# Optimization experiments

Hardware: AMD Instinct MI355X
Metric: run time of the kernel (lower is better)

The kernel has to match this reference:

```python
import jax, jax.numpy as jnp
import numpy as np

N = 100000      # nodes
E = 1600000     # edges
D_IN = 128
D_OUT = 64
D_EDGE = 2
NEG_SLOPE = 0.01  # F.leaky_relu default


def setup_inputs() -> dict:
    key = jax.random.key(0)
    ks = jax.random.split(key, 8)
    h = jax.random.normal(ks[0], (N, D_IN), dtype=jnp.float32)
    e = jax.random.normal(ks[1], (E, D_EDGE), dtype=jnp.float32)
    src = jax.random.randint(ks[2], (E,), 0, N, dtype=jnp.int32)
    dst = jax.random.randint(ks[3], (E,), 0, N, dtype=jnp.int32)
    # learned params (torch Linear stores [out, in]; y = x @ W.T)
    W_fc = jax.random.normal(ks[4], (D_OUT, D_IN), dtype=jnp.float32) * 0.05
    W_attn = jax.random.normal(ks[5], (1, 2 * D_OUT + D_EDGE), dtype=jnp.float32) * 0.05
    W_edge = jax.random.normal(ks[6], (D_EDGE, D_EDGE), dtype=jnp.float32) * 0.5
    W_e2n = jax.random.normal(ks[7], (D_OUT, D_EDGE), dtype=jnp.float32) * 0.5
    return {"h": h, "e": e, "src": src, "dst": dst,
            "W_fc": W_fc, "W_attn": W_attn, "W_edge": W_edge, "W_e2n": W_e2n}


def reference(h, e, src, dst, W_fc, W_attn, W_edge, W_e2n):
    z = h @ W_fc.T                    # [N, D_OUT]
    ex = e @ W_edge.T                 # [E, D_EDGE]
    ez = ex @ W_e2n.T                 # [E, D_OUT]
    # edge attention logit: attn_fc(concat[z_src, z_dst, ex]) then leaky_relu
    z_src = z[src]                    # [E, D_OUT]
    z_dst = z[dst]                    # [E, D_OUT]
    wa = W_attn[0]                    # [2*D_OUT + D_EDGE]
    a = (z_src @ wa[:D_OUT] + z_dst @ wa[D_OUT:2 * D_OUT]
         + ex @ wa[2 * D_OUT:])       # [E]
    a = jnp.where(a > 0, a, NEG_SLOPE * a)
    # segment softmax over incoming edges of each dst node
    m = jax.ops.segment_max(a, dst, num_segments=N)      # [N]
    m = jnp.where(jnp.isfinite(m), m, 0.0)               # isolated nodes
    a_exp = jnp.exp(a - m[dst])                          # [E]
    denom = jax.ops.segment_sum(a_exp, dst, num_segments=N)  # [N]
    attn = a_exp / denom[dst]                            # [E]
    # h = sum attn * z_src + sum attn * ez  (fused)
    msg = attn[:, None] * (z_src + ez)                   # [E, D_OUT]
    h_out = jax.ops.segment_sum(msg, dst, num_segments=N)  # [N, D_OUT]
    return h_out
```

## Files before the change

### kernel.cpp

```cpp
#include <hip/hip_runtime.h>
#include <hip/hip_fp16.h>
#include <math.h>

#define D_IN 128
#define D_OUT 64
#define NEG_SLOPE 0.01f

#define NBIN 391
#define BSH  8
#define FCAP 6144
#define ECH  2048
#define ETH  512
#define EPT  4
#define CSLOT 48

typedef __attribute__((ext_vector_type(8))) short bf16x8;
typedef __attribute__((ext_vector_type(4))) float f32x4;

static __device__ __forceinline__ unsigned short f2bf(float f) {
    unsigned u = __float_as_uint(f);
    u += 0x7FFFu + ((u >> 16) & 1u);
    return (unsigned short)(u >> 16);
}
static __device__ __forceinline__ float h2f(unsigned bits) {
    __half_raw r; r.x = (unsigned short)bits;
    return __half2float(__half(r));
}
static __device__ __forceinline__ float i8b(unsigned w, int b) {
    return (float)((int)(w << (24 - 8 * b)) >> 24);
}

__global__ __launch_bounds__(256) void k_prep(const float* __restrict__ W_fc,
                                              unsigned short* __restrict__ Wf)
{
    int t = threadIdx.x;
    for (int idx = t; idx < 8192; idx += 256) {
        int j  = idx & 7;
        int l  = (idx >> 3) & 63;
        int ks = (idx >> 9) & 3;
        int ct = idx >> 11;
        int col = ct * 16 + (l & 15);
        int k   = ks * 32 + (l >> 4) * 8 + j;
        Wf[idx] = f2bf(W_fc[col * 128 + k]);
    }
}

__global__ __launch_bounds__(256) void k_z(const float* __restrict__ h,
                                           const unsigned short* __restrict__ Wf,
                                           const float* __restrict__ W_attn,
                                           unsigned* __restrict__ zq,
                                           float* __restrict__ sc1f,
                                           float* __restrict__ s2,
                                           int N)
{
    __shared__ __align__(16) char smem[64 * 68 * 4];
    unsigned short* fr = (unsigned short*)smem;
    float* zt = (float*)smem;

    int t = threadIdx.x;
    int row0 = blockIdx.x * 64;

#pragma unroll
    for (int it = 0; it < 8; ++it) {
        int idx = it * 256 + t;
        int row = idx >> 5, kq = idx & 31;
        int rw = row0 + row;
        float4 v = (rw < N) ? *(const float4*)&h[(size_t)rw * D_IN + kq * 4]
                            : make_float4(0.f, 0.f, 0.f, 0.f);
        ushort4 b;
        b.x = f2bf(v.x); b.y = f2bf(v.y); b.z = f2bf(v.z); b.w = f2bf(v.w);
        int m = kq >> 1;
        int rt = row >> 4, r16 = row & 15;
        int eidx = (rt * 16 + m) * 128 + ((r16 ^ (m & 7)) * 8) + (kq & 1) * 4;
        *(ushort4*)&fr[eidx] = b;
    }
    __syncthreads();

    int w = t >> 6, l = t & 63;
    int kg = l >> 4, r16 = l & 15;

    bf16x8 A[4];
#pragma unroll
    for (int ks = 0; ks < 4; ++ks) {
        int m = ks * 4 + kg;
        A[ks] = *(const bf16x8*)&fr[(w * 16 + m) * 128 + ((r16 ^ (m & 7)) * 8)];
    }
    f32x4 acc[4];
#pragma unroll
    for (int ct = 0; ct < 4; ++ct) {
        acc[ct] = (f32x4){0.f, 0.f, 0.f, 0.f};
#pragma unroll
        for (int ks = 0; ks < 4; ++ks) {
            bf16x8 B = *(const bf16x8*)&Wf[((ct * 4 + ks) * 64 + l) * 8];
            acc[ct] = __builtin_amdgcn_mfma_f32_16x16x32_bf16(A[ks], B, acc[ct], 0, 0, 0);
        }
    }
    __syncthreads();

#pragma unroll
    for (int ct = 0; ct < 4; ++ct)
#pragma unroll
        for (int j = 0; j < 4; ++j)
            zt[(w * 16 + kg * 4 + j) * 68 + ct * 16 + r16] = acc[ct][j];
    __syncthreads();

    int tx = t & 15, ty = t >> 4;
    float a4[4][4];
#pragma unroll
    for (int i = 0; i < 4; i++) {
        float4 vv = *(const float4*)&zt[(ty * 4 + i) * 68 + tx * 4];
        a4[i][0] = vv.x; a4[i][1] = vv.y; a4[i][2] = vv.z; a4[i][3] = vv.w;
    }

#pragma unroll
    for (int i = 0; i < 4; i++) {
        float m = fmaxf(fmaxf(fabsf(a4[i][0]), fabsf(a4[i][1])),
                        fmaxf(fabsf(a4[i][2]), fabsf(a4[i][3])));
#pragma unroll
        for (int msk = 8; msk >= 1; msk >>= 1)
            m = fmaxf(m, __shfl_xor(m, msk));
        float inv = (m > 0.0f) ? 127.0f / m : 0.0f;
        int q0 = __float2int_rn(a4[i][0] * inv);
        int q1 = __float2int_rn(a4[i][1] * inv);
        int q2 = __float2int_rn(a4[i][2] * inv);
        int q3 = __float2int_rn(a4[i][3] * inv);
        q0 = min(127, max(-127, q0)); q1 = min(127, max(-127, q1));
        q2 = min(127, max(-127, q2)); q3 = min(127, max(-127, q3));
        unsigned pk = ((unsigned)(q0 & 255)) | ((unsigned)(q1 & 255) << 8)
                    | ((unsigned)(q2 & 255) << 16) | ((unsigned)(q3 & 255) << 24);
        int row = row0 + ty * 4 + i;
        if (row < N) {
            zq[(size_t)row * 16 + tx] = pk;
            if (tx == 0) sc1f[2 * row] = m * (1.0f / 127.0f);
        }
    }

    float4 wa0 = *(const float4*)&W_attn[tx * 4];
    float4 wa1 = *(const float4*)&W_attn[64 + tx * 4];
#pragma unroll
    for (int i = 0; i < 4; i++) {
        float v1 = a4[i][0] * wa0.x + a4[i][1] * wa0.y + a4[i][2] * wa0.z + a4[i][3] * wa0.w;
        float v2 = a4[i][0] * wa1.x + a4[i][1] * wa1.y + a4[i][2] * wa1.z + a4[i][3] * wa1.w;
#pragma unroll
        for (int msk = 8; msk >= 1; msk >>= 1) {
            v1 += __shfl_xor(v1, msk);
            v2 += __shfl_xor(v2, msk);
        }
        if (tx == 0) {
            int row = row0 + ty * 4 + i;
            if (row < N) { sc1f[2 * row + 1] = v1; s2[row] = v2; }
        }
    }
}

__global__ __launch_bounds__(ETH) void k_edge_bin(const float2* __restrict__ e,
                                                  const int* __restrict__ src,
                                                  const int* __restrict__ dst,
                                                  const float* __restrict__ W_edge,
                                                  const float* __restrict__ W_attn,
                                                  int* __restrict__ fifo_tail,
                                                  unsigned* __restrict__ f0,
                                                  unsigned* __restrict__ f1,
                                                  unsigned char* __restrict__ fD,
                                                  int E)
{
    __shared__ unsigned l0[ECH];
    __shared__ unsigned l1[ECH];
    __shared__ unsigned char ldl[ECH];
    __shared__ unsigned short lbin[ECH];
    __shared__ int cnt[NBIN];
    __shared__ int off[NBIN + 1];
    __shared__ int gbase[NBIN];
    __shared__ int wsum[ETH / 64];

    int t = threadIdx.x;
    int base = blockIdx.x * ECH;

    for (int i = t; i < NBIN; i += ETH) cnt[i] = 0;
    __syncthreads();

    float we0 = W_edge[0], we1 = W_edge[1], we2 = W_edge[2], we3 = W_edge[3];
    float wa0 = W_attn[128], wa1 = W_attn[129];
    float v0c = we0 * wa0 + we2 * wa1;
    float v1c = we1 * wa0 + we3 * wa1;

    unsigned r0[EPT], r1[EPT];
    unsigned char rdl[EPT];
    int rbin[EPT], rrank[EPT];

#pragma unroll
    for (int j = 0; j < EPT; j++) {
        int i = base + j * ETH + t;
        bool ok = (i < E);
        int ii = ok ? i : 0;
        float2 ev = e[ii];
        int s = src[ii], d = dst[ii];
        float a = ev.x * v0c + ev.y * v1c;
        float a2 = fminf(fmaxf(a + 2.0f, 0.0f), 4.0f);
        if (ok) {
            int b = d >> BSH;
            rrank[j] = atomicAdd(&cnt[b], 1);
            rbin[j] = b;
            unsigned pb = __half_as_ushort(__float2half_rn(a2)) & 0x7FFFu;
            r0[j] = ((unsigned)s << 15) | pb;
            unsigned e0b = __half_as_ushort(__float2half_rn(ev.x));
            unsigned e1b = __half_as_ushort(__float2half_rn(ev.y));
            r1[j] = (e0b << 16) | e1b;
            rdl[j] = (unsigned char)(d & 255);
        } else {
            rbin[j] = -1;
        }
    }
    __syncthreads();

    {
        int i0 = 2 * t, i1 = 2 * t + 1;
        int a0 = (i0 < NBIN) ? cnt[i0] : 0;
        int a1 = (i1 < NBIN) ? cnt[i1] : 0;
        int tsum = a0 + a1;
        int lane = t & 63, w = t >> 6;
        int sc = tsum;
#pragma unroll
        for (int o = 1; o < 64; o <<= 1) {
            int u = __shfl_up(sc, o);
            if (lane >= o) sc += u;
        }
        if (lane == 63) wsum[w] = sc;
        __syncthreads();
        int woff = 0;
        for (int ww = 0; ww < w; ww++) woff += wsum[ww];
        int ex = woff + sc - tsum;
        if (i0 <= NBIN) off[i0] = ex;
        if (i1 <= NBIN) off[i1] = ex + a0;
        __syncthreads();
    }

#pragma unroll
    for (int j = 0; j < EPT; j++) {
        if (rbin[j] >= 0) {
            int slot = off[rbin[j]] + rrank[j];
            l0[slot] = r0[j];
            l1[slot] = r1[j];
            ldl[slot] = rdl[j];
            lbin[slot] = (unsigned short)rbin[j];
        }
    }

    for (int i = t; i < NBIN; i += ETH) {
        int c = cnt[i];
        gbase[i] = (c > 0) ? atomicAdd(&fifo_tail[i], c) : 0;
    }
    __syncthreads();

    int total = off[NBIN];
    for (int r = t; r < total; r += ETH) {
        int b = lbin[r];
        int gi = gbase[b] + (r - off[b]);
        if (gi < FCAP) {
            size_t a = (size_t)b * FCAP + gi;
            f0[a] = l0[r];
            f1[a] = l1[r];
            fD[a] = ldl[r];
        }
    }
}

__global__ __launch_bounds__(256) void k_bin2slot(const int* __restrict__ fifo_tail,
                                                  const unsigned* __restrict__ f0,
                                                  const unsigned* __restrict__ f1,
                                                  const unsigned char* __restrict__ fD,
                                                  int* __restrict__ gcur,
                                                  uint2* __restrict__ slots, int N)
{
    __shared__ int cnt[256];
    __shared__ int gb[256];
    __shared__ unsigned short rk[(FCAP + 1) / 2];

    int b = blockIdx.x >> 1;
    int half = blockIdx.x & 1;
    int t = threadIdx.x;

    int cnt0 = fifo_tail[b];
    if (cnt0 > FCAP) cnt0 = FCAP;
    int mid = (cnt0 + 1) >> 1;
    int lo = half ? mid : 0;
    int hi = half ? cnt0 : mid;

    cnt[t] = 0;
    __syncthreads();

    size_t fb = (size_t)b * FCAP;
    for (int idx = lo + t; idx < hi; idx += 256) {
        int dl = fD[fb + idx];
        rk[idx - lo] = (unsigned short)atomicAdd(&cnt[dl], 1);
    }
    __syncthreads();

    {
        int c = cnt[t];
        int node = b * 256 + t;
        gb[t] = (c > 0 && node < N) ? atomicAdd(&gcur[node], c) : 0;
    }
    __syncthreads();

    for (int idx = lo + t; idx < hi; idx += 256) {
        int dl = fD[fb + idx];
        int pos = gb[dl] + (int)rk[idx - lo];
        if (pos < CSLOT) {
            int node = b * 256 + dl;
            slots[(size_t)node * CSLOT + pos] = make_uint2(f0[fb + idx], f1[fb + idx]);
        }
    }
}

__global__ __launch_bounds__(256) void k_node2(const unsigned* __restrict__ zq,
                                               const float2* __restrict__ sc1,
                                               const uint2* __restrict__ slots,
                                               const int* __restrict__ deg,
                                               const float* __restrict__ s2,
                                               const float* __restrict__ W_edge,
                                               const float* __restrict__ W_e2n,
                                               float* __restrict__ out, int N)
{
    int wid = threadIdx.x >> 6, lane = threadIdx.x & 63;
    int hh = lane >> 5, hl = lane & 31;
    int hb = hh << 5;
    int n = blockIdx.x * 8 + wid * 2 + hh;
    bool valid = (n < N);
    int nn = valid ? n : 0;
    size_t base = (size_t)nn * CSLOT;

    uint2 v = slots[base + hl];
    int cnt = deg[nn];
    float s2n = s2[nn] - 2.0f;
    if (!valid) cnt = 0;
    if (cnt > CSLOT) cnt = CSLOT;
    int c32 = cnt < 32 ? cnt : 32;

    unsigned v0 = v.x;
    float p = 0.0f, ps = 0.0f, pe0 = 0.0f, pe1 = 0.0f;
    if (hl < c32) {
        float2 sv = sc1[v.x >> 15];
        float af = h2f(v.x & 0x7FFFu) + sv.y + s2n;
        af = af > 0.0f ? af : NEG_SLOPE * af;
        p = __expf(af);
        ps = p * sv.x;
        pe0 = p * h2f(v.y >> 16);
        pe1 = p * h2f(v.y & 0xFFFFu);
    } else {
        v0 = 0;
    }

    int sub4 = hl & 15, qq = hl >> 4;
    float acc0 = 0.0f, acc1 = 0.0f, acc2 = 0.0f, acc3 = 0.0f;

    int k = 0;
    for (; k + 8 <= c32; k += 8) {
        unsigned aa[4]; float pb[4];
#pragma unroll
        for (int j = 0; j < 4; j++) {
            int kk = hb + k + 2 * j + qq;
            aa[j] = __shfl(v0, kk);
            pb[j] = __shfl(ps, kk);
        }
        unsigned w[4];
#pragma unroll
        for (int j = 0; j < 4; j++)
            w[j] = zq[(size_t)(aa[j] >> 15) * 16 + sub4];
#pragma unroll
        for (int j = 0; j < 4; j++) {
            acc0 = fmaf(pb[j], i8b(w[j], 0), acc0);
            acc1 = fmaf(pb[j], i8b(w[j], 1), acc1);
            acc2 = fmaf(pb[j], i8b(w[j], 2), acc2);
            acc3 = fmaf(pb[j], i8b(w[j], 3), acc3);
        }
    }
    for (; k < c32; k += 2) {
        int kk = hb + k + qq;
        unsigned aa = __shfl(v0, kk);
        float pb = __shfl(ps, kk);
        unsigned w = zq[(size_t)(aa >> 15) * 16 + sub4];
        acc0 = fmaf(pb, i8b(w, 0), acc0);
        acc1 = fmaf(pb, i8b(w, 1), acc1);
        acc2 = fmaf(pb, i8b(w, 2), acc2);
        acc3 = fmaf(pb, i8b(w, 3), acc3);
    }

    if (__any(cnt > 32)) {
        uint2 v2 = slots[base + 32 + (size_t)(hl & 15)];
        unsigned u0 = 0;
        float ps2 = 0.0f;
        if (hl < 16 && 32 + hl < cnt) {
            float2 sv = sc1[v2.x >> 15];
            float af = h2f(v2.x & 0x7FFFu) + sv.y + s2n;
            af = af > 0.0f ? af : NEG_SLOPE * af;
            float p2 = __expf(af);
            ps2 = p2 * sv.x;
            p   += p2;
            pe0 += p2 * h2f(v2.y >> 16);
            pe1 += p2 * h2f(v2.y & 0xFFFFu);
            u0 = v2.x;
        }
        for (int k2 = 0; k2 < 16; k2 += 2) {
            int kk = hb + k2 + qq;
            unsigned aa = __shfl(u0, kk);
            float pb = __shfl(ps2, kk);
            unsigned w = zq[(size_t)(aa >> 15) * 16 + sub4];
            acc0 = fmaf(pb, i8b(w, 0), acc0);
            acc1 = fmaf(pb, i8b(w, 1), acc1);
            acc2 = fmaf(pb, i8b(w, 2), acc2);
            acc3 = fmaf(pb, i8b(w, 3), acc3);
        }
    }

    acc0 += __shfl_xor(acc0, 16);
    acc1 += __shfl_xor(acc1, 16);
    acc2 += __shfl_xor(acc2, 16);
    acc3 += __shfl_xor(acc3, 16);
#pragma unroll
    for (int msk = 16; msk >= 1; msk >>= 1) {
        p   += __shfl_xor(p, msk);
        pe0 += __shfl_xor(pe0, msk);
        pe1 += __shfl_xor(pe1, msk);
    }

    if (valid && hl < 16) {
        float4 r = make_float4(0.f, 0.f, 0.f, 0.f);
        if (cnt > 0 && p > 0.0f) {
            float we0 = W_edge[0], we1 = W_edge[1], we2 = W_edge[2], we3 = W_edge[3];
            float4 wnA = *(const float4*)&W_e2n[8 * sub4];
            float4 wnB = *(const float4*)&W_e2n[8 * sub4 + 4];
            float ex0 = we0 * pe0 + we1 * pe1;
            float ex1 = we2 * pe0 + we3 * pe1;
            float inv = 1.0f / p;
            r.x = (acc0 + wnA.x * ex0 + wnA.y * ex1) * inv;
            r.y = (acc1 + wnA.z * ex0 + wnA.w * ex1) * inv;
            r.z = (acc2 + wnB.x * ex0 + wnB.y * ex1) * inv;
            r.w = (acc3 + wnB.z * ex0 + wnB.w * ex1) * inv;
        }
        *(float4*)&out[(size_t)n * 64 + 4 * sub4] = r;
    }
}

__global__ __launch_bounds__(256) void k_count(const int* __restrict__ dst,
                                               int* __restrict__ counts, int E)
{
    int i = blockIdx.x * 256 + threadIdx.x;
    if (i < E) atomicAdd(&counts[dst[i]], 1);
}

__global__ __launch_bounds__(256) void k_scan1(const int* __restrict__ counts,
                                               int* __restrict__ tmp,
                                               int* __restrict__ partials, int N)
{
    __shared__ int wsum[4];
    int b = blockIdx.x, t = threadIdx.x;
    int base = b * 1024 + t * 4;
    int v[4];
#pragma unroll
    for (int j = 0; j < 4; j++) { int i = base + j; v[j] = (i < N) ? counts[i] : 0; }
    int tsum = v[0] + v[1] + v[2] + v[3];
    int lane = t & 63, w = t >> 6;
    int sc = tsum;
#pragma unroll
    for (int off = 1; off < 64; off <<= 1) {
        int u = __shfl_up(sc, off);
        if (lane >= off) sc += u;
    }
    if (lane == 63) wsum[w] = sc;
    __syncthreads();
    int woff = 0;
    for (int ww = 0; ww < w; ww++) woff += wsum[ww];
    int ex = woff + sc - tsum;
#pragma unroll
    for (int j = 0; j < 4; j++) { int i = base + j; if (i < N) tmp[i] = ex; ex += v[j]; }
    if (t == 255) partials[b] = woff + sc;
}

__global__ __launch_bounds__(128) void k_scan2(const int* __restrict__ partials,
                                               int* __restrict__ blockoff,
                                               int* __restrict__ offsets,
                                               int NB, int N)
{
    __shared__ int lds[128];
    int t = threadIdx.x;
    int v = (t < NB) ? partials[t] : 0;
    lds[t] = v;
    __syncthreads();
    for (int off = 1; off < 128; off <<= 1) {
        int u = (t >= off) ? lds[t - off] : 0;
        __syncthreads();
        lds[t] += u;
        __syncthreads();
    }
    if (t < NB) blockoff[t] = lds[t] - v;
    if (t == 0) offsets[N] = lds[127];
}

__global__ __launch_bounds__(256) void k_scan3(const int* __restrict__ tmp,
                                               const int* __restrict__ blockoff,
                                               int* __restrict__ offsets,
                                               int* __restrict__ cursor, int N)
{
    int i = blockIdx.x * 256 + threadIdx.x;
    if (i < N) {
        int o = tmp[i] + blockoff[i >> 10];
        offsets[i] = o;
        cursor[i] = o;
    }
}

__global__ __launch_bounds__(256) void k_edge_csr(const float2* __restrict__ e,
                                                  const int* __restrict__ src,
                                                  const int* __restrict__ dst,
                                                  const float* __restrict__ W_edge,
                                                  const float* __restrict__ W_attn,
                                                  const float2* __restrict__ sc1,
                                                  const float* __restrict__ s2,
                                                  int* __restrict__ cursor,
                                                  int4* __restrict__ csr, int E)
{
    int i = blockIdx.x * 256 + threadIdx.x;
    if (i >= E) return;
    float2 ev = e[i];
    float ex0 = ev.x * W_edge[0] + ev.y * W_edge[1];
    float ex1 = ev.x * W_edge[2] + ev.y * W_edge[3];
    int s = src[i], d = dst[i];
    float a = sc1[s].y + s2[d] + ex0 * W_attn[128] + ex1 * W_attn[129];
    a = a > 0.0f ? a : NEG_SLOPE * a;
    float p = __expf(a);
    int pos = atomicAdd(&cursor[d], 1);
    csr[pos] = make_int4(s, __float_as_int(p), __float_as_int(ex0), __float_as_int(ex1));
}

__global__ __launch_bounds__(256) void k_node_csr(const unsigned char* __restrict__ zq8,
                                                  const float2* __restrict__ sc1,
                                                  const int4* __restrict__ recs,
                                                  const int* __restrict__ meta,
                                                  const float* __restrict__ W_e2n,
                                                  float* __restrict__ out, int N)
{
    int wid = threadIdx.x >> 6, lane = threadIdx.x & 63;
    int n = blockIdx.x * 4 + wid;
    if (n >= N) return;

    int o0 = meta[n];
    int cnt = meta[n + 1] - o0;
    size_t base = (size_t)o0;

    float acc = 0.0f, pl = 0.0f, px = 0.0f, py = 0.0f;

    for (int c0 = 0; c0 < cnt; c0 += 64) {
        int m = cnt - c0;
        if (m > 64) m = 64;
        int4 v = make_int4(0, 0, 0, 0);
        if (lane < m) v = recs[base + c0 + lane];

        float pown = __int_as_float(v.y);
        pl += pown;
        px = fmaf(pown, __int_as_float(v.z), px);
        py = fmaf(pown, __int_as_float(v.w), py);

        for (int k = 0; k < m; ++k) {
            int s = __shfl(v.x, k);
            float p = __int_as_float(__shfl(v.y, k));
            float sc = sc1[s].x;
            float zf = (float)((int)(signed char)zq8[(size_t)s * 64 + lane]) * sc;
            acc = fmaf(p, zf, acc);
        }
    }

#pragma unroll
    for (int msk = 32; msk >= 1; msk >>= 1) {
        pl += __shfl_xor(pl, msk);
        px += __shfl_xor(px, msk);
        py += __shfl_xor(py, msk);
    }
    float w0 = W_e2n[2 * lane], w1 = W_e2n[2 * lane + 1];
    float res = (cnt > 0) ? (acc + px * w0 + py * w1) / pl : 0.0f;
    out[(size_t)n * 64 + lane] = res;
}

extern "C" void kernel_launch(void* const* d_in, const int* in_sizes, int n_in,
                              void* d_out, int out_size, void* d_ws, size_t ws_size,
                              hipStream_t stream)
{
    const float*  h      = (const float*)d_in[0];
    const float2* e      = (const float2*)d_in[1];
    const int*    src    = (const int*)d_in[2];
    const int*    dst    = (const int*)d_in[3];
    const float*  W_fc   = (const float*)d_in[4];
    const float*  W_attn = (const float*)d_in[5];
    const float*  W_edge = (const float*)d_in[6];
    const float*  W_e2n  = (const float*)d_in[7];
    float* out = (float*)d_out;

    int N = in_sizes[0] / D_IN;
    int E = in_sizes[2];

    char* ws = (char*)d_ws;
    size_t o = 0;
    auto alloc = [&](size_t bytes) -> void* {
        void* p = ws + o;
        o += (bytes + 255) & ~(size_t)255;
        return p;
    };

    unsigned* zq  = (unsigned*)alloc((size_t)N * 64);
    float2* sc1   = (float2*)alloc((size_t)N * 8);
    float* s2     = (float*)alloc((size_t)N * 4);
    unsigned short* Wf = (unsigned short*)alloc(8192 * 2);
    int*   gcur = (int*)alloc((size_t)N * 4);
    size_t fixed_end = o;

    int zbk = (N + 63) / 64;

    size_t need = (size_t)NBIN * 4
                + 2 * ((size_t)NBIN * FCAP * 4)
                + (size_t)NBIN * FCAP
                + (size_t)N * CSLOT * 8 + 8192;

    if (N == 100000 && E <= 1600000 && ws_size >= fixed_end + need) {
        int* fifo_tail = (int*)alloc((size_t)NBIN * 4);
        unsigned* f0 = (unsigned*)alloc((size_t)NBIN * FCAP * 4);
        unsigned* f1 = (unsigned*)alloc((size_t)NBIN * FCAP * 4);
        unsigned char* fD = (unsigned char*)alloc((size_t)NBIN * FCAP);
        uint2* slots = (uint2*)alloc((size_t)N * CSLOT * 8);

        hipMemsetAsync(gcur, 0, (size_t)N * 4, stream);
        hipMemsetAsync(fifo_tail, 0, (size_t)NBIN * 4, stream);

        k_prep<<<1, 256, 0, stream>>>(W_fc, Wf);
        k_z<<<zbk, 256, 0, stream>>>(h, Wf, W_attn, zq, (float*)sc1, s2, N);

        int ebb = (E + ECH - 1) / ECH;
        k_edge_bin<<<ebb, ETH, 0, stream>>>(e, src, dst, W_edge, W_attn,
                                            fifo_tail, f0, f1, fD, E);

        k_bin2slot<<<NBIN * 2, 256, 0, stream>>>(fifo_tail, f0, f1, fD,
                                                 gcur, slots, N);

        int nnb = (N + 7) / 8;
        k_node2<<<nnb, 256, 0, stream>>>(zq, sc1, slots, gcur, s2,
                                         W_edge, W_e2n, out, N);
    } else {
        int* counts   = (int*)alloc((size_t)N * 4);
        int* tmp      = (int*)alloc((size_t)N * 4);
        int* offsets  = (int*)alloc((size_t)(N + 1) * 4);
        int* partials = (int*)alloc(1024 * 4);
        int* blockoff = (int*)alloc(1024 * 4);
        int4* csr     = (int4*)alloc((size_t)E * 16);

        hipMemsetAsync(counts, 0, (size_t)N * 4, stream);
        k_prep<<<1, 256, 0, stream>>>(W_fc, Wf);
        k_z<<<zbk, 256, 0, stream>>>(h, Wf, W_attn, zq, (float*)sc1, s2, N);
        int eb = (E + 255) / 256;
        k_count<<<eb, 256, 0, stream>>>(dst, counts, E);
        int NB = (N + 1023) / 1024;
        k_scan1<<<NB, 256, 0, stream>>>(counts, tmp, partials, N);
        k_scan2<<<1, 128, 0, stream>>>(partials, blockoff, offsets, NB, N);
        int nb3 = (N + 255) / 256;
        k_scan3<<<nb3, 256, 0, stream>>>(tmp, blockoff, offsets, gcur, N);
        k_edge_csr<<<eb, 256, 0, stream>>>(e, src, dst, W_edge, W_attn,
                                           sc1, s2, gcur, csr, E);
        int nnb = (N + 3) / 4;
        k_node_csr<<<nnb, 256, 0, stream>>>((const unsigned char*)zq, sc1,
                                            csr, offsets, W_e2n, out, N);
    }
}
```

Measured before the change: 123.8 us.

## Merge node transform and edge binning into one interleaved kernel launch

Combines the z-projection kernel and the edge-binning kernel into a single launch whose blocks alternate between two 64-row z tiles and one edge chunk, sharing one statically sized LDS buffer. Because the two stages are independent, the aim is to overlap the compute-heavy MFMA work with the memory- and atomic-heavy binning and to drop one launch boundary. The bin-to-slot kernel also moves to 512 threads per block so each block processes its half-bin with more threads. In exchange, z blocks now run at 512 threads with a larger LDS footprint, which may lower occupancy, and the hand-computed LDS offsets must stay consistent with the original array sizes.

```diff
diff --git a/kernel.cpp b/kernel.cpp
--- a/kernel.cpp
+++ b/kernel.cpp
@@ -13,6 +13,7 @@
 #define ETH  512
 #define EPT  4
 #define CSLOT 48
+#define ZT_BYTES 17408
 
 typedef __attribute__((ext_vector_type(8))) short bf16x8;
 typedef __attribute__((ext_vector_type(4))) float f32x4;
@@ -45,24 +46,21 @@
     }
 }
 
-__global__ __launch_bounds__(256) void k_z(const float* __restrict__ h,
-                                           const unsigned short* __restrict__ Wf,
-                                           const float* __restrict__ W_attn,
-                                           unsigned* __restrict__ zq,
-                                           float* __restrict__ sc1f,
-                                           float* __restrict__ s2,
-                                           int N)
-{
-    __shared__ __align__(16) char smem[64 * 68 * 4];
-    unsigned short* fr = (unsigned short*)smem;
-    float* zt = (float*)smem;
-
-    int t = threadIdx.x;
-    int row0 = blockIdx.x * 64;
+static __device__ __forceinline__
+void z_tile_body(const float* __restrict__ h,
+                 const unsigned short* __restrict__ Wf,
+                 const float* __restrict__ W_attn,
+                 unsigned* __restrict__ zq,
+                 float* __restrict__ sc1f,
+                 float* __restrict__ s2,
+                 int N, char* sm, int t2, int row0)
+{
+    unsigned short* fr = (unsigned short*)sm;
+    float* zt = (float*)sm;
 
 #pragma unroll
     for (int it = 0; it < 8; ++it) {
-        int idx = it * 256 + t;
+        int idx = it * 256 + t2;
         int row = idx >> 5, kq = idx & 31;
         int rw = row0 + row;
         float4 v = (rw < N) ? *(const float4*)&h[(size_t)rw * D_IN + kq * 4]
@@ -76,7 +74,7 @@
     }
     __syncthreads();
 
-    int w = t >> 6, l = t & 63;
+    int w = t2 >> 6, l = t2 & 63;
     int kg = l >> 4, r16 = l & 15;
 
     bf16x8 A[4];
@@ -104,7 +102,7 @@
             zt[(w * 16 + kg * 4 + j) * 68 + ct * 16 + r16] = acc[ct][j];
     __syncthreads();
 
-    int tx = t & 15, ty = t >> 4;
+    int tx = t2 & 15, ty = t2 >> 4;
     float a4[4][4];
 #pragma unroll
     for (int i = 0; i < 4; i++) {
@@ -153,28 +151,53 @@
     }
 }
 
-__global__ __launch_bounds__(ETH) void k_edge_bin(const float2* __restrict__ e,
-                                                  const int* __restrict__ src,
-                                                  const int* __restrict__ dst,
-                                                  const float* __restrict__ W_edge,
-                                                  const float* __restrict__ W_attn,
-                                                  int* __restrict__ fifo_tail,
-                                                  unsigned* __restrict__ f0,
-                                                  unsigned* __restrict__ f1,
-                                                  unsigned char* __restrict__ fD,
-                                                  int E)
-{
-    __shared__ unsigned l0[ECH];
-    __shared__ unsigned l1[ECH];
-    __shared__ unsigned char ldl[ECH];
-    __shared__ unsigned short lbin[ECH];
-    __shared__ int cnt[NBIN];
-    __shared__ int off[NBIN + 1];
-    __shared__ int gbase[NBIN];
-    __shared__ int wsum[ETH / 64];
+__global__ __launch_bounds__(ETH) void k_ze(const float* __restrict__ h,
+                                            const unsigned short* __restrict__ Wf,
+                                            const float* __restrict__ W_attn,
+                                            unsigned* __restrict__ zq,
+                                            float* __restrict__ sc1f,
+                                            float* __restrict__ s2,
+                                            const float2* __restrict__ e,
+                                            const int* __restrict__ src,
+                                            const int* __restrict__ dst,
+                                            const float* __restrict__ W_edge,
+                                            int* __restrict__ fifo_tail,
+                                            unsigned* __restrict__ f0,
+                                            unsigned* __restrict__ f1,
+                                            unsigned char* __restrict__ fD,
+                                            int N, int E, int nz, int ne)
+{
+    __shared__ __align__(16) char smem[2 * ZT_BYTES];
+
+    int bid = blockIdx.x;
+    int m2 = 2 * (nz < ne ? nz : ne);
+    bool isZ; int id;
+    if (bid < m2) { isZ = !(bid & 1); id = bid >> 1; }
+    else {
+        int r = bid - m2;
+        if (nz > ne) { isZ = true;  id = ne + r; }
+        else         { isZ = false; id = nz + r; }
+    }
 
     int t = threadIdx.x;
-    int base = blockIdx.x * ECH;
+
+    if (isZ) {
+        int tile = t >> 8, t2 = t & 255;
+        z_tile_body(h, Wf, W_attn, zq, sc1f, s2, N,
+                    smem + tile * ZT_BYTES, t2, id * 128 + tile * 64);
+        return;
+    }
+
+    unsigned* l0 = (unsigned*)smem;
+    unsigned* l1 = (unsigned*)(smem + 8192);
+    unsigned char* ldl = (unsigned char*)(smem + 16384);
+    unsigned short* lbin = (unsigned short*)(smem + 18432);
+    int* cnt   = (int*)(smem + 22528);
+    int* off   = (int*)(smem + 24096);
+    int* gbase = (int*)(smem + 25664);
+    int* wsum  = (int*)(smem + 27232);
+
+    int base = id * ECH;
 
     for (int i = t; i < NBIN; i += ETH) cnt[i] = 0;
     __syncthreads();
@@ -265,7 +288,7 @@
     }
 }
 
-__global__ __launch_bounds__(256) void k_bin2slot(const int* __restrict__ fifo_tail,
+__global__ __launch_bounds__(512) void k_bin2slot(const int* __restrict__ fifo_tail,
                                                   const unsigned* __restrict__ f0,
                                                   const unsigned* __restrict__ f1,
                                                   const unsigned char* __restrict__ fD,
@@ -286,24 +309,24 @@
     int lo = half ? mid : 0;
     int hi = half ? cnt0 : mid;
 
-    cnt[t] = 0;
+    if (t < 256) cnt[t] = 0;
     __syncthreads();
 
     size_t fb = (size_t)b * FCAP;
-    for (int idx = lo + t; idx < hi; idx += 256) {
+    for (int idx = lo + t; idx < hi; idx += 512) {
         int dl = fD[fb + idx];
         rk[idx - lo] = (unsigned short)atomicAdd(&cnt[dl], 1);
     }
     __syncthreads();
 
-    {
+    if (t < 256) {
         int c = cnt[t];
         int node = b * 256 + t;
         gb[t] = (c > 0 && node < N) ? atomicAdd(&gcur[node], c) : 0;
     }
     __syncthreads();
 
-    for (int idx = lo + t; idx < hi; idx += 256) {
+    for (int idx = lo + t; idx < hi; idx += 512) {
         int dl = fD[fb + idx];
         int pos = gb[dl] + (int)rk[idx - lo];
         if (pos < CSLOT) {
@@ -442,6 +465,18 @@
     }
 }
 
+__global__ __launch_bounds__(256) void k_z(const float* __restrict__ h,
+                                           const unsigned short* __restrict__ Wf,
+                                           const float* __restrict__ W_attn,
+                                           unsigned* __restrict__ zq,
+                                           float* __restrict__ sc1f,
+                                           float* __restrict__ s2,
+                                           int N)
+{
+    __shared__ __align__(16) char smem[ZT_BYTES];
+    z_tile_body(h, Wf, W_attn, zq, sc1f, s2, N, smem, threadIdx.x, blockIdx.x * 64);
+}
+
 __global__ __launch_bounds__(256) void k_count(const int* __restrict__ dst,
                                                int* __restrict__ counts, int E)
 {
@@ -613,8 +648,6 @@
     int*   gcur = (int*)alloc((size_t)N * 4);
     size_t fixed_end = o;
 
-    int zbk = (N + 63) / 64;
-
     size_t need = (size_t)NBIN * 4
                 + 2 * ((size_t)NBIN * FCAP * 4)
                 + (size_t)NBIN * FCAP
@@ -631,13 +664,14 @@
         hipMemsetAsync(fifo_tail, 0, (size_t)NBIN * 4, stream);
 
         k_prep<<<1, 256, 0, stream>>>(W_fc, Wf);
-        k_z<<<zbk, 256, 0, stream>>>(h, Wf, W_attn, zq, (float*)sc1, s2, N);
-
-        int ebb = (E + ECH - 1) / ECH;
-        k_edge_bin<<<ebb, ETH, 0, stream>>>(e, src, dst, W_edge, W_attn,
-                                            fifo_tail, f0, f1, fD, E);
-
-        k_bin2slot<<<NBIN * 2, 256, 0, stream>>>(fifo_tail, f0, f1, fD,
+
+        int nz = (N + 127) / 128;
+        int ne = (E + ECH - 1) / ECH;
+        k_ze<<<nz + ne, ETH, 0, stream>>>(h, Wf, W_attn, zq, (float*)sc1, s2,
+                                          e, src, dst, W_edge,
+                                          fifo_tail, f0, f1, fD, N, E, nz, ne);
+
+        k_bin2slot<<<NBIN * 2, 512, 0, stream>>>(fifo_tail, f0, f1, fD,
                                                  gcur, slots, N);
 
         int nnb = (N + 7) / 8;
@@ -653,6 +687,7 @@
 
         hipMemsetAsync(counts, 0, (size_t)N * 4, stream);
         k_prep<<<1, 256, 0, stream>>>(W_fc, Wf);
+        int zbk = (N + 63) / 64;
         k_z<<<zbk, 256, 0, stream>>>(h, Wf, W_attn, zq, (float*)sc1, s2, N);
         int eb = (E + 255) / 256;
         k_count<<<eb, 256, 0, stream>>>(dst, counts, E);
```

Result: faster. 109.2 us, median of 2 (-11.8%).
